# Kernel tuning notes

Hardware: AMD Instinct MI355X
Metric: run time of the kernel (lower is better)

Reference implementation:

```python
import jax, jax.numpy as jnp
import numpy as np

ALPHA = 0.2  # LeakyReLU negative slope
MASK_VAL = -9e15


def setup_inputs() -> dict:
    key = jax.random.key(0)
    k1, k2, k3, k4 = jax.random.split(key, 4)
    B, N, F_IN = 4, 2048, 256
    H, HD = 8, 32  # out_features = H*HD = 256
    x = jax.random.normal(k1, (B, N, F_IN), dtype=jnp.float32)
    adj = jax.random.randint(k2, (B, N, N), 0, 2, dtype=jnp.int32)
    W = jax.random.normal(k3, (H, F_IN, HD), dtype=jnp.float32) * (1.0 / np.sqrt(F_IN))
    a = jax.random.normal(k4, (H, 2 * HD, 1), dtype=jnp.float32) * 0.1
    return {"x": x, "adj": adj, "W": W, "a": a}


def reference(x, adj, W, a):
    # x: (B,N,F), W: (H,F,D), a: (H,2D,1)
    B, N, _ = x.shape
    H, _, D = W.shape
    Wh = jnp.einsum('bnf,hfd->bhnd', x, W)  # (B,H,N,D)
    # Split additive attention vector: cat([Wh_i, Wh_j]) @ a == Wh_i@a1 + Wh_j@a2
    a1 = a[:, :D, 0]   # (H,D)
    a2 = a[:, D:, 0]   # (H,D)
    s1 = jnp.einsum('bhnd,hd->bhn', Wh, a1)  # source scores
    s2 = jnp.einsum('bhnd,hd->bhn', Wh, a2)  # target scores
    e = jax.nn.leaky_relu(s1[:, :, :, None] + s2[:, :, None, :], negative_slope=ALPHA)  # (B,H,N,N)
    e = jnp.where(adj[:, None, :, :] == 0, MASK_VAL, e)
    attention = jax.nn.softmax(e, axis=-1)  # dropout skipped (eval mode)
    h = jnp.einsum('bhij,bhjd->bhid', attention, Wh)  # (B,H,N,D)
    h = jnp.transpose(h, (0, 2, 1, 3)).reshape(B, N, H * D)
    return jax.nn.elu(h)
```

## Files before the change

### kernel.cpp

```cpp
#include <hip/hip_runtime.h>
#include <hip/hip_bf16.h>

#define ALPHA 0.2f

typedef __attribute__((ext_vector_type(8))) short short8;
typedef __attribute__((ext_vector_type(4))) short s4;
typedef __attribute__((ext_vector_type(8))) _Float16 h8;
typedef __attribute__((ext_vector_type(2))) _Float16 h2v;
typedef __attribute__((ext_vector_type(4))) float f32x4;
typedef __attribute__((ext_vector_type(2))) short sh2;

static constexpr int B = 4, N = 2048, F = 256, H = 8, D = 32;
static constexpr int SZ_X = B * N * F, SZ_ADJ = B * N * N, SZ_W = H * F * D, SZ_A = H * 2 * D;
static const float C1 = 1.4426950408889634f;
static const float C2 = ALPHA * 1.4426950408889634f;


__device__ __forceinline__ unsigned rne16(unsigned u) {
    return u + 0x7fffu + ((u >> 16) & 1u);
}
__device__ __forceinline__ unsigned pk_rne(float a, float b) {
    return __builtin_amdgcn_perm(rne16(__float_as_uint(b)),
                                 rne16(__float_as_uint(a)), 0x07060302u);
}
__device__ __forceinline__ unsigned h2mul(unsigned a, unsigned b) {
    h2v r = __builtin_bit_cast(h2v, a) * __builtin_bit_cast(h2v, b);
    return __builtin_bit_cast(unsigned, r);
}
__device__ __forceinline__ unsigned h2max(unsigned a, unsigned b) {
    h2v r = __builtin_elementwise_max(__builtin_bit_cast(h2v, a),
                                      __builtin_bit_cast(h2v, b));
    return __builtin_bit_cast(unsigned, r);
}
__device__ __forceinline__ unsigned dup16f(float x) {
    unsigned short w = __builtin_bit_cast(unsigned short, (_Float16)x);
    return (unsigned)w | ((unsigned)w << 16);
}
__device__ __forceinline__ unsigned bits2mask(unsigned mk, unsigned mulc) {
    unsigned w = (mk & 3u) * mulc;
    sh2 s = __builtin_bit_cast(sh2, w);
    s = s >> 15;
    return __builtin_bit_cast(unsigned, s);
}

__global__ void k0_prep(const float* __restrict__ Wp, const float* __restrict__ ap,
                        unsigned short* __restrict__ WT2, float* __restrict__ AF) {
    int bid = blockIdx.x;
    int h = bid >> 5, d = bid & 31;
    int f = threadIdx.x;
    unsigned short v = (unsigned short)(rne16(__float_as_uint(Wp[(h * F + f) * D + d])) >> 16);
    WT2[(size_t)(f >> 5) * 8192 + (h * 32 + d) * 32 + (f & 31)] = v;
    if (d == 0 && f < 64) AF[h * 64 + f] = ap[h * 64 + f];
}

__global__ __launch_bounds__(256, 4) void k2_fused(const float* __restrict__ x,
                                                   const unsigned short* __restrict__ WT2,
                                                   const float* __restrict__ AF,
                                                   unsigned short* __restrict__ WHT,
                                                   float* __restrict__ S1,
                                                   _Float16* __restrict__ UH,
                                                   _Float16* __restrict__ VH,
                                                   const int* __restrict__ adj,
                                                   unsigned long long* __restrict__ bm) {
    __shared__ unsigned short XA[16 * 264];
    int bid = blockIdx.x;
    int rr = bid % 5;
    int grp = bid / 5;
    int t = threadIdx.x;

    if (rr != 4) {
        int wid = (grp * 4 + rr) * 4 + (t >> 6);
        int lane = t & 63;
        size_t base = (size_t)wid * 32;
        const int* ap2 = adj + base * 64 + lane;
        int v0[16], v1[16];
#pragma unroll
        for (int s = 0; s < 16; s++) v0[s] = ap2[(size_t)s * 64];
#pragma unroll
        for (int s = 0; s < 16; s++) v1[s] = ap2[(size_t)(16 + s) * 64];
        unsigned long long m0[16];
#pragma unroll
        for (int s = 0; s < 16; s++) m0[s] = __ballot(v0[s] != 0);
        unsigned long long m1[16];
#pragma unroll
        for (int s = 0; s < 16; s++) m1[s] = __ballot(v1[s] != 0);
        if (lane == 0) {
#pragma unroll
            for (int s = 0; s < 16; s++) bm[base + s] = m0[s];
#pragma unroll
            for (int s = 0; s < 16; s++) bm[base + 16 + s] = m1[s];
        }
        return;
    }

    int b = grp >> 7;
    int n0 = (grp & 127) * 16;
    int wave = t >> 6, lane = t & 63;
    int lm = lane & 15, lq = lane >> 4;

#pragma unroll
    for (int q = 0; q < 4; q++) {
        int idx = q * 256 + t;
        int row = idx >> 6, c16 = idx & 63;
        f32x4 v = *(const f32x4*)(x + (size_t)(b * N + n0 + row) * F + c16 * 4);
        unsigned* dst = (unsigned*)&XA[row * 264 + c16 * 4];
        dst[0] = pk_rne(v[0], v[1]);
        dst[1] = pk_rne(v[2], v[3]);
    }

    short8 bcur[4], bnext[4];
#pragma unroll
    for (int c = 0; c < 4; c++)
        bcur[c] = *(const short8*)(WT2 + (size_t)(wave * 64 + c * 16 + lm) * 32 + lq * 8);
    __syncthreads();

    f32x4 acc[4] = {};
#pragma unroll
    for (int kc = 0; kc < 8; kc++) {
        if (kc < 7) {
#pragma unroll
            for (int c = 0; c < 4; c++)
                bnext[c] = *(const short8*)(WT2 + (size_t)(kc + 1) * 8192 +
                                            (wave * 64 + c * 16 + lm) * 32 + lq * 8);
        }
        short8 afr = *(const short8*)&XA[lm * 264 + kc * 32 + lq * 8];
#pragma unroll
        for (int c = 0; c < 4; c++)
            acc[c] = __builtin_amdgcn_mfma_f32_16x16x32_bf16(afr, bcur[c], acc[c], 0, 0, 0);
#pragma unroll
        for (int c = 0; c < 4; c++) bcur[c] = bnext[c];
    }

#pragma unroll
    for (int c = 0; c < 4; c++) {
        int hd = wave * 64 + c * 16 + lm;
        unsigned short w0 = __builtin_bit_cast(unsigned short, (_Float16)acc[c][0]);
        unsigned short w1 = __builtin_bit_cast(unsigned short, (_Float16)acc[c][1]);
        unsigned short w2 = __builtin_bit_cast(unsigned short, (_Float16)acc[c][2]);
        unsigned short w3 = __builtin_bit_cast(unsigned short, (_Float16)acc[c][3]);
        uint2 pk;
        pk.x = (unsigned)w0 | ((unsigned)w1 << 16);
        pk.y = (unsigned)w2 | ((unsigned)w3 << 16);
        *(uint2*)&WHT[((size_t)b * 256 + hd) * 2048 + n0 + lq * 4] = pk;
    }
#pragma unroll
    for (int cp = 0; cp < 2; cp++) {
        int h = wave * 2 + cp;
        float a1l = AF[h * 64 + lm],      a1h = AF[h * 64 + 16 + lm];
        float a2l = AF[h * 64 + 32 + lm], a2h = AF[h * 64 + 48 + lm];
#pragma unroll
        for (int r = 0; r < 4; r++) {
            float s1p = acc[cp * 2][r] * a1l + acc[cp * 2 + 1][r] * a1h;
            float s2p = acc[cp * 2][r] * a2l + acc[cp * 2 + 1][r] * a2h;
#pragma unroll
            for (int off = 1; off <= 8; off <<= 1) {
                s1p += __shfl_xor(s1p, off);
                s2p += __shfl_xor(s2p, off);
            }
            if (lm == 0) {
                int bh = b * 8 + h, n = n0 + lq * 4 + r;
                S1[(size_t)bh * 2048 + n] = s1p;
                UH[(size_t)bh * 2048 + n] = (_Float16)exp2f(C1 * s2p);
                VH[(size_t)bh * 2048 + n] = (_Float16)exp2f(C2 * s2p);
            }
        }
    }
}

__global__ __launch_bounds__(256) void k3_attn(
    const unsigned* __restrict__ bm32,
    const unsigned short* __restrict__ WHT,
    const float* __restrict__ S1,
    const _Float16* __restrict__ UH, const _Float16* __restrict__ VH,
    float* __restrict__ out) {
    __shared__ unsigned LM[4][32 * 66];
    __shared__ unsigned short LW[4][32 * 140];

    int bid = blockIdx.x;
    int bh = (bid & 7) + ((bid >> 7) << 3);
    int isup = (bid >> 3) & 15;
    int b = bh >> 3, h = bh & 7;
    int i0 = isup * 128;
    int t = threadIdx.x;
    int wave = t >> 6, lane = t & 63;
    int irow = lane & 15, quad = lane >> 4;
    int iw = i0 + wave * 32;

    {
        unsigned* lmp = LM[wave];
        const unsigned* src = bm32 + ((size_t)(b * N + iw)) * 64;
#pragma unroll
        for (int r = 0; r < 32; r++)
            lmp[r * 66 + lane] = src[(size_t)r * 64 + lane];
    }

    const unsigned short* wsrc = WHT + ((size_t)b * 256 + h * 32) * 2048;
    int srow = t >> 3, sseg = (t & 7) * 16;

    {
        const unsigned short* g0 = wsrc + (size_t)srow * 2048 + sseg;
        union { short8 v; s4 q[2]; } a0, c0, a1, c1;
        a0.v = *(const short8*)(g0);
        c0.v = *(const short8*)(g0 + 8);
        a1.v = *(const short8*)(g0 + 128);
        c1.v = *(const short8*)(g0 + 136);
        unsigned short* d0 = &LW[0][srow * 140 + sseg];
        *(s4*)(d0) = a0.q[0]; *(s4*)(d0 + 4) = a0.q[1];
        *(s4*)(d0 + 8) = c0.q[0]; *(s4*)(d0 + 12) = c0.q[1];
        unsigned short* d1 = &LW[1][srow * 140 + sseg];
        *(s4*)(d1) = a1.q[0]; *(s4*)(d1 + 4) = a1.q[1];
        *(s4*)(d1 + 8) = c1.q[0]; *(s4*)(d1 + 12) = c1.q[1];
    }

    float s1A = S1[(size_t)bh * 2048 + iw + irow];
    float s1B = S1[(size_t)bh * 2048 + iw + 16 + irow];
    unsigned ci2A = dup16f(exp2f((C2 - C1) * s1A));
    unsigned ci2B = dup16f(exp2f((C2 - C1) * s1B));
    const _Float16* up = UH + (size_t)bh * 2048;
    const _Float16* vp = VH + (size_t)bh * 2048;

    union { h8 v; unsigned u[4]; } ones;
    ones.u[0] = ones.u[1] = ones.u[2] = ones.u[3] = 0x3C003C00u;

    const unsigned MUL = 0x40008000u;

    f32x4 aA0 = {0,0,0,0}, aA1 = {0,0,0,0}, aAL = {0,0,0,0};
    f32x4 aB0 = {0,0,0,0}, aB1 = {0,0,0,0}, aBL = {0,0,0,0};
    __syncthreads();

    for (int g = 0; g < 8; g++) {
        union { short8 v; s4 q[2]; } pa0, pc0, pa1, pc1;
        if (g < 7) {
            const unsigned short* g0 = wsrc + (size_t)srow * 2048 + (2 * g + 2) * 128 + sseg;
            pa0.v = *(const short8*)(g0);
            pc0.v = *(const short8*)(g0 + 8);
            pa1.v = *(const short8*)(g0 + 128);
            pc1.v = *(const short8*)(g0 + 136);
        }
        const unsigned* lmw = LM[wave];
#pragma unroll
        for (int ci = 0; ci < 2; ci++) {
            int cc = 2 * g + ci;
            const unsigned short* lwp = LW[cc & 3];
#pragma unroll
            for (int ks = 0; ks < 4; ks++) {
                int jl = ks * 32 + quad * 8;
                int jg = cc * 128 + jl;
                uint4 uw = *(const uint4*)(up + jg);
                uint4 vw = *(const uint4*)(vp + jg);
                unsigned mkA = lmw[irow * 66 + cc * 4 + ks] >> (quad * 8);
                unsigned mkB = lmw[(16 + irow) * 66 + cc * 4 + ks] >> (quad * 8);
                unsigned mA0 = bits2mask(mkA,      MUL);
                unsigned mA1 = bits2mask(mkA >> 2, MUL);
                unsigned mA2 = bits2mask(mkA >> 4, MUL);
                unsigned mA3 = bits2mask(mkA >> 6, MUL);
                unsigned mB0 = bits2mask(mkB,      MUL);
                unsigned mB1 = bits2mask(mkB >> 2, MUL);
                unsigned mB2 = bits2mask(mkB >> 4, MUL);
                unsigned mB3 = bits2mask(mkB >> 6, MUL);
                union { h8 v; unsigned u[4]; } afA, afB;
                afA.u[0] = h2max(uw.x, h2mul(ci2A, vw.x)) & mA0;
                afA.u[1] = h2max(uw.y, h2mul(ci2A, vw.y)) & mA1;
                afA.u[2] = h2max(uw.z, h2mul(ci2A, vw.z)) & mA2;
                afA.u[3] = h2max(uw.w, h2mul(ci2A, vw.w)) & mA3;
                afB.u[0] = h2max(uw.x, h2mul(ci2B, vw.x)) & mB0;
                afB.u[1] = h2max(uw.y, h2mul(ci2B, vw.y)) & mB1;
                afB.u[2] = h2max(uw.z, h2mul(ci2B, vw.z)) & mB2;
                afB.u[3] = h2max(uw.w, h2mul(ci2B, vw.w)) & mB3;
                union { short8 v; s4 q[2]; } bf0, bf1;
                bf0.q[0] = *(const s4*)&lwp[irow * 140 + jl];
                bf0.q[1] = *(const s4*)&lwp[irow * 140 + jl + 4];
                bf1.q[0] = *(const s4*)&lwp[(16 + irow) * 140 + jl];
                bf1.q[1] = *(const s4*)&lwp[(16 + irow) * 140 + jl + 4];
                h8 b0 = __builtin_bit_cast(h8, bf0.v);
                h8 b1 = __builtin_bit_cast(h8, bf1.v);
                aA0 = __builtin_amdgcn_mfma_f32_16x16x32_f16(afA.v, b0, aA0, 0, 0, 0);
                aA1 = __builtin_amdgcn_mfma_f32_16x16x32_f16(afA.v, b1, aA1, 0, 0, 0);
                aAL = __builtin_amdgcn_mfma_f32_16x16x32_f16(afA.v, ones.v, aAL, 0, 0, 0);
                aB0 = __builtin_amdgcn_mfma_f32_16x16x32_f16(afB.v, b0, aB0, 0, 0, 0);
                aB1 = __builtin_amdgcn_mfma_f32_16x16x32_f16(afB.v, b1, aB1, 0, 0, 0);
                aBL = __builtin_amdgcn_mfma_f32_16x16x32_f16(afB.v, ones.v, aBL, 0, 0, 0);
            }
        }
        if (g < 7) {
            unsigned short* d0 = &LW[(2 * g + 2) & 3][srow * 140 + sseg];
            *(s4*)(d0) = pa0.q[0]; *(s4*)(d0 + 4) = pa0.q[1];
            *(s4*)(d0 + 8) = pc0.q[0]; *(s4*)(d0 + 12) = pc0.q[1];
            unsigned short* d1 = &LW[(2 * g + 3) & 3][srow * 140 + sseg];
            *(s4*)(d1) = pa1.q[0]; *(s4*)(d1 + 4) = pa1.q[1];
            *(s4*)(d1 + 8) = pc1.q[0]; *(s4*)(d1 + 12) = pc1.q[1];
        }
        __syncthreads();
    }

#pragma unroll
    for (int r = 0; r < 4; r++) {
        float lA = aAL[r], lB = aBL[r];
        float rA = 1.0f / (lA > 0.f ? lA : 1.f);
        float rB = 1.0f / (lB > 0.f ? lB : 1.f);
        float vA0 = aA0[r] * rA, vA1 = aA1[r] * rA;
        float vB0 = aB0[r] * rB, vB1 = aB1[r] * rB;
        vA0 = vA0 > 0.f ? vA0 : __expf(vA0) - 1.f;
        vA1 = vA1 > 0.f ? vA1 : __expf(vA1) - 1.f;
        vB0 = vB0 > 0.f ? vB0 : __expf(vB0) - 1.f;
        vB1 = vB1 > 0.f ? vB1 : __expf(vB1) - 1.f;
        int iA = iw + quad * 4 + r, iB = iA + 16;
        size_t rbA = (size_t)(b * N + iA) * 256 + h * 32;
        size_t rbB = (size_t)(b * N + iB) * 256 + h * 32;
        out[rbA + irow] = vA0;
        out[rbA + 16 + irow] = vA1;
        out[rbB + irow] = vB0;
        out[rbB + 16 + irow] = vB1;
    }
}

extern "C" void kernel_launch(void* const* d_in, const int* in_sizes, int n_in,
                              void* d_out, int out_size, void* d_ws, size_t ws_size,
                              hipStream_t stream) {
    const void *xP = nullptr, *adjP = nullptr, *WP = nullptr, *aP = nullptr;
    for (int i = 0; i < n_in; i++) {
        switch (in_sizes[i]) {
            case SZ_X:   xP = d_in[i]; break;
            case SZ_ADJ: adjP = d_in[i]; break;
            case SZ_W:   WP = d_in[i]; break;
            case SZ_A:   aP = d_in[i]; break;
            default: break;
        }
    }
    if (!xP || !adjP || !WP || !aP) { xP = d_in[0]; adjP = d_in[1]; WP = d_in[2]; aP = d_in[3]; }
    float* out = (float*)d_out;

    char* ws = (char*)d_ws;
    unsigned short* WT2 = (unsigned short*)(ws);
    float* AF  = (float*)(ws + 131072);
    float* S1  = (float*)(ws + 133120);
    _Float16* UH = (_Float16*)(ws + 395264);
    _Float16* VH = (_Float16*)(ws + 526336);
    unsigned short* WHT = (unsigned short*)(ws + 657408);
    unsigned long long* BM = (unsigned long long*)(ws + 4851712);

    k0_prep<<<256, 256, 0, stream>>>((const float*)WP, (const float*)aP, WT2, AF);
    k2_fused<<<2560, 256, 0, stream>>>((const float*)xP, WT2, AF, WHT, S1, UH, VH,
                                       (const int*)adjP, BM);
    k3_attn<<<512, 256, 0, stream>>>((const unsigned*)BM, WHT, S1, UH, VH, out);
}
```

Measured before the change: 141.6 us.

## Halve rows per wave in attention kernel and double grid size

The attention kernel now has each wave handle 16 query rows instead of 32, so each block covers 64 rows and the grid doubles to 1024 blocks. Mask words are loaded from LDS as one 128-bit read per chunk, and the UH/VH vectors are batched ahead of the MFMA loop. This raises parallelism and cuts register pressure, which should help occupancy. The cost is that the WHT tile staged in LDS, and the UH/VH loads, are now reused across half as many rows, so global and LDS traffic per output roughly doubles.

```diff
diff --git a/kernel.cpp b/kernel.cpp
--- a/kernel.cpp
+++ b/kernel.cpp
@@ -173,25 +173,25 @@
     const float* __restrict__ S1,
     const _Float16* __restrict__ UH, const _Float16* __restrict__ VH,
     float* __restrict__ out) {
-    __shared__ unsigned LM[4][32 * 66];
+    __shared__ unsigned LM[4][16 * 68];
     __shared__ unsigned short LW[4][32 * 140];
 
     int bid = blockIdx.x;
-    int bh = (bid & 7) + ((bid >> 7) << 3);
-    int isup = (bid >> 3) & 15;
+    int bh = (bid & 7) + ((bid >> 8) << 3);
+    int tile = (bid >> 3) & 31;
     int b = bh >> 3, h = bh & 7;
-    int i0 = isup * 128;
+    int i0 = tile * 64;
     int t = threadIdx.x;
     int wave = t >> 6, lane = t & 63;
     int irow = lane & 15, quad = lane >> 4;
-    int iw = i0 + wave * 32;
+    int iw = i0 + wave * 16;
 
     {
         unsigned* lmp = LM[wave];
         const unsigned* src = bm32 + ((size_t)(b * N + iw)) * 64;
 #pragma unroll
-        for (int r = 0; r < 32; r++)
-            lmp[r * 66 + lane] = src[(size_t)r * 64 + lane];
+        for (int r = 0; r < 16; r++)
+            lmp[r * 68 + lane] = src[(size_t)r * 64 + lane];
     }
 
     const unsigned short* wsrc = WHT + ((size_t)b * 256 + h * 32) * 2048;
@@ -213,9 +213,7 @@
     }
 
     float s1A = S1[(size_t)bh * 2048 + iw + irow];
-    float s1B = S1[(size_t)bh * 2048 + iw + 16 + irow];
     unsigned ci2A = dup16f(exp2f((C2 - C1) * s1A));
-    unsigned ci2B = dup16f(exp2f((C2 - C1) * s1B));
     const _Float16* up = UH + (size_t)bh * 2048;
     const _Float16* vp = VH + (size_t)bh * 2048;
 
@@ -225,7 +223,6 @@
     const unsigned MUL = 0x40008000u;
 
     f32x4 aA0 = {0,0,0,0}, aA1 = {0,0,0,0}, aAL = {0,0,0,0};
-    f32x4 aB0 = {0,0,0,0}, aB1 = {0,0,0,0}, aBL = {0,0,0,0};
     __syncthreads();
 
     for (int g = 0; g < 8; g++) {
@@ -242,31 +239,27 @@
         for (int ci = 0; ci < 2; ci++) {
             int cc = 2 * g + ci;
             const unsigned short* lwp = LW[cc & 3];
+            uint4 mkq = *(const uint4*)&lmw[irow * 68 + cc * 4];
+            unsigned mkw[4] = { mkq.x, mkq.y, mkq.z, mkq.w };
+            uint4 uws[4], vws[4];
+#pragma unroll
+            for (int ks = 0; ks < 4; ks++) {
+                uws[ks] = *(const uint4*)(up + cc * 128 + ks * 32 + quad * 8);
+                vws[ks] = *(const uint4*)(vp + cc * 128 + ks * 32 + quad * 8);
+            }
 #pragma unroll
             for (int ks = 0; ks < 4; ks++) {
                 int jl = ks * 32 + quad * 8;
-                int jg = cc * 128 + jl;
-                uint4 uw = *(const uint4*)(up + jg);
-                uint4 vw = *(const uint4*)(vp + jg);
-                unsigned mkA = lmw[irow * 66 + cc * 4 + ks] >> (quad * 8);
-                unsigned mkB = lmw[(16 + irow) * 66 + cc * 4 + ks] >> (quad * 8);
+                unsigned mkA = mkw[ks] >> (quad * 8);
                 unsigned mA0 = bits2mask(mkA,      MUL);
                 unsigned mA1 = bits2mask(mkA >> 2, MUL);
                 unsigned mA2 = bits2mask(mkA >> 4, MUL);
                 unsigned mA3 = bits2mask(mkA >> 6, MUL);
-                unsigned mB0 = bits2mask(mkB,      MUL);
-                unsigned mB1 = bits2mask(mkB >> 2, MUL);
-                unsigned mB2 = bits2mask(mkB >> 4, MUL);
-                unsigned mB3 = bits2mask(mkB >> 6, MUL);
-                union { h8 v; unsigned u[4]; } afA, afB;
-                afA.u[0] = h2max(uw.x, h2mul(ci2A, vw.x)) & mA0;
-                afA.u[1] = h2max(uw.y, h2mul(ci2A, vw.y)) & mA1;
-                afA.u[2] = h2max(uw.z, h2mul(ci2A, vw.z)) & mA2;
-                afA.u[3] = h2max(uw.w, h2mul(ci2A, vw.w)) & mA3;
-                afB.u[0] = h2max(uw.x, h2mul(ci2B, vw.x)) & mB0;
-                afB.u[1] = h2max(uw.y, h2mul(ci2B, vw.y)) & mB1;
-                afB.u[2] = h2max(uw.z, h2mul(ci2B, vw.z)) & mB2;
-                afB.u[3] = h2max(uw.w, h2mul(ci2B, vw.w)) & mB3;
+                union { h8 v; unsigned u[4]; } afA;
+                afA.u[0] = h2max(uws[ks].x, h2mul(ci2A, vws[ks].x)) & mA0;
+                afA.u[1] = h2max(uws[ks].y, h2mul(ci2A, vws[ks].y)) & mA1;
+                afA.u[2] = h2max(uws[ks].z, h2mul(ci2A, vws[ks].z)) & mA2;
+                afA.u[3] = h2max(uws[ks].w, h2mul(ci2A, vws[ks].w)) & mA3;
                 union { short8 v; s4 q[2]; } bf0, bf1;
                 bf0.q[0] = *(const s4*)&lwp[irow * 140 + jl];
                 bf0.q[1] = *(const s4*)&lwp[irow * 140 + jl + 4];
@@ -277,9 +270,6 @@
                 aA0 = __builtin_amdgcn_mfma_f32_16x16x32_f16(afA.v, b0, aA0, 0, 0, 0);
                 aA1 = __builtin_amdgcn_mfma_f32_16x16x32_f16(afA.v, b1, aA1, 0, 0, 0);
                 aAL = __builtin_amdgcn_mfma_f32_16x16x32_f16(afA.v, ones.v, aAL, 0, 0, 0);
-                aB0 = __builtin_amdgcn_mfma_f32_16x16x32_f16(afB.v, b0, aB0, 0, 0, 0);
-                aB1 = __builtin_amdgcn_mfma_f32_16x16x32_f16(afB.v, b1, aB1, 0, 0, 0);
-                aBL = __builtin_amdgcn_mfma_f32_16x16x32_f16(afB.v, ones.v, aBL, 0, 0, 0);
             }
         }
         if (g < 7) {
@@ -295,22 +285,15 @@
 
 #pragma unroll
     for (int r = 0; r < 4; r++) {
-        float lA = aAL[r], lB = aBL[r];
+        float lA = aAL[r];
         float rA = 1.0f / (lA > 0.f ? lA : 1.f);
-        float rB = 1.0f / (lB > 0.f ? lB : 1.f);
         float vA0 = aA0[r] * rA, vA1 = aA1[r] * rA;
-        float vB0 = aB0[r] * rB, vB1 = aB1[r] * rB;
         vA0 = vA0 > 0.f ? vA0 : __expf(vA0) - 1.f;
         vA1 = vA1 > 0.f ? vA1 : __expf(vA1) - 1.f;
-        vB0 = vB0 > 0.f ? vB0 : __expf(vB0) - 1.f;
-        vB1 = vB1 > 0.f ? vB1 : __expf(vB1) - 1.f;
-        int iA = iw + quad * 4 + r, iB = iA + 16;
+        int iA = iw + quad * 4 + r;
         size_t rbA = (size_t)(b * N + iA) * 256 + h * 32;
-        size_t rbB = (size_t)(b * N + iB) * 256 + h * 32;
         out[rbA + irow] = vA0;
         out[rbA + 16 + irow] = vA1;
-        out[rbB + irow] = vB0;
-        out[rbB + 16 + irow] = vB1;
     }
 }
 
@@ -342,5 +325,5 @@
     k0_prep<<<256, 256, 0, stream>>>((const float*)WP, (const float*)aP, WT2, AF);
     k2_fused<<<2560, 256, 0, stream>>>((const float*)xP, WT2, AF, WHT, S1, UH, VH,
                                        (const int*)adjP, BM);
-    k3_attn<<<512, 256, 0, stream>>>((const unsigned*)BM, WHT, S1, UH, VH, out);
-}
+    k3_attn<<<1024, 256, 0, stream>>>((const unsigned*)BM, WHT, S1, UH, VH, out);
+}
```

After: 146.8 us. +3.7%, slower.
